# Optimization experiments

Hardware: AMD Instinct MI355X
Metric: run time of the kernel (lower is better)

The kernel has to match this reference:

```python
import jax, jax.numpy as jnp
import numpy as np

B, S, D = 2, 2048, 2048
H, HKV = 32, 8
DH = D // H          # 64
G = H // HKV         # group size 4


def setup_inputs() -> dict:
    key = jax.random.key(0)
    ks = jax.random.split(key, 5)
    sc = lambda fan_in: 1.0 / np.sqrt(fan_in)
    return {
        "hidden_states": jax.random.normal(ks[0], (B, S, D), jnp.float32),
        "Wq": jax.random.normal(ks[1], (D, D), jnp.float32) * sc(D),
        "bq": jnp.zeros((D,), jnp.float32),
        "Wk": jax.random.normal(ks[2], (D, HKV * DH), jnp.float32) * sc(D),
        "bk": jnp.zeros((HKV * DH,), jnp.float32),
        "Wv": jax.random.normal(ks[3], (D, HKV * DH), jnp.float32) * sc(D),
        "bv": jnp.zeros((HKV * DH,), jnp.float32),
        "Wo": jax.random.normal(ks[4], (D, D), jnp.float32) * sc(D),
        "bo": jnp.zeros((D,), jnp.float32),
    }


def reference(hidden_states, Wq, bq, Wk, bk, Wv, bv, Wo, bo):
    x = hidden_states
    # projections
    q = x @ Wq + bq                     # [B,S,D]
    k = x @ Wk + bk                     # [B,S,HKV*DH]
    v = x @ Wv + bv
    # split heads; group queries so K/V broadcast instead of repeat_interleave
    # (same math: repeat_interleave expands kv head j to query heads j*G..j*G+G-1)
    q = q.reshape(B, S, HKV, G, DH).transpose(0, 2, 3, 1, 4)  # [B,HKV,G,S,DH]
    k = k.reshape(B, S, HKV, DH).transpose(0, 2, 1, 3)        # [B,HKV,S,DH]
    v = v.reshape(B, S, HKV, DH).transpose(0, 2, 1, 3)
    scale = 1.0 / jnp.sqrt(jnp.asarray(DH, q.dtype))
    scores = jnp.einsum('bhgqd,bhkd->bhgqk', q, k) * scale    # [B,HKV,G,S,S]
    attn = jax.nn.softmax(scores, axis=-1)
    ctx = jnp.einsum('bhgqk,bhkd->bhgqd', attn, v)            # [B,HKV,G,S,DH]
    # merge heads back to [B,S,D] (head order = kv_head*G + group idx)
    merged = ctx.transpose(0, 3, 1, 2, 4).reshape(B, S, D)
    out = merged @ Wo + bo
    return out
```

## Files before the change

kernel.cpp:

```cpp
#include <hip/hip_runtime.h>
#include <cstdint>

typedef __bf16 bf16;
typedef __attribute__((ext_vector_type(8))) __bf16 bf16x8;
typedef __attribute__((ext_vector_type(4))) __bf16 bf16x4;
typedef __attribute__((ext_vector_type(2))) __bf16 bf16x2;
typedef __attribute__((ext_vector_type(4))) float f32x4;
typedef __attribute__((ext_vector_type(16))) float f32x16;

#define B_   2
#define S_   2048
#define D_   2048
#define HKV_ 8
#define H_   32
#define DH_  64

__device__ __forceinline__ void async_cp16(const bf16* g, bf16* l) {
  __builtin_amdgcn_global_load_lds(
      (__attribute__((address_space(1))) void*)g,
      (__attribute__((address_space(3))) void*)l,
      16, 0, 0);
}

__device__ __forceinline__ float fexp2(float x) {
#if __has_builtin(__builtin_amdgcn_exp2f)
  return __builtin_amdgcn_exp2f(x);
#else
  return __expf(x * 0.69314718056f);
#endif
}

__global__ __launch_bounds__(256) void downcast_k(
    const float* __restrict__ in, bf16* __restrict__ out, int n8) {
  const int i = blockIdx.x * 256 + threadIdx.x;
  if (i < n8) {
    const float4* p = (const float4*)(in + (size_t)i * 8);
    const float4 lo = p[0];
    const float4 hi = p[1];
    bf16x8 v;
    v[0] = (bf16)lo.x; v[1] = (bf16)lo.y; v[2] = (bf16)lo.z; v[3] = (bf16)lo.w;
    v[4] = (bf16)hi.x; v[5] = (bf16)hi.y; v[6] = (bf16)hi.z; v[7] = (bf16)hi.w;
    *(bf16x8*)(out + (size_t)i * 8) = v;
  }
}

__global__ __launch_bounds__(256) void transpose_k(
    const float* __restrict__ in, bf16* __restrict__ out, int R, int C) {
  __shared__ bf16 tile[64][65];
  const int tx = threadIdx.x & 63;
  const int ty = threadIdx.x >> 6;
  const int r0 = blockIdx.x * 64;
  const int c0 = blockIdx.y * 64;
#pragma unroll
  for (int j = 0; j < 16; ++j) {
    int r = j * 4 + ty;
    tile[r][tx] = (bf16)in[(size_t)(r0 + r) * C + c0 + tx];
  }
  __syncthreads();
#pragma unroll
  for (int j = 0; j < 16; ++j) {
    int r = j * 4 + ty;
    out[(size_t)(c0 + r) * R + r0 + tx] = tile[tx][r];
  }
}

template <int OMODE>
__global__ __launch_bounds__(256) void gemm_bt(
    const bf16* __restrict__ A, const bf16* __restrict__ Bt,
    const float* __restrict__ b1, const float* __restrict__ b2,
    const float* __restrict__ b3,
    void* __restrict__ C0, void* __restrict__ C1, void* __restrict__ C2,
    int N, int K) {
  __shared__ bf16 a_tile[128 * 64];
  __shared__ bf16 b_tile[128 * 64];
  const int tid  = threadIdx.x;
  const int wave = tid >> 6;
  const int lane = tid & 63;
  const int quad = lane >> 4;
  const int l16  = lane & 15;
  const int m0   = blockIdx.x * 128;
  const int n0   = blockIdx.y * 128;
  const int wm   = (wave >> 1) * 64;
  const int wn   = (wave & 1) * 64;

  f32x4 acc[4][4] = {};

  const int srow  = wave * 32 + (lane >> 3);
  const int skoff = (lane & 7) * 8;
  const bf16* Ag = A  + (size_t)(m0 + srow) * K + skoff;
  const bf16* Bg = Bt + (size_t)(n0 + srow) * K + skoff;
  bf16* al = &a_tile[srow * 64 + skoff];
  bf16* bl = &b_tile[srow * 64 + skoff];

  for (int kt = 0; kt < K; kt += 64) {
    __syncthreads();
#pragma unroll
    for (int c = 0; c < 4; ++c)
      async_cp16(Ag + (size_t)(c * 8) * K + kt, al + c * 512);
#pragma unroll
    for (int c = 0; c < 4; ++c)
      async_cp16(Bg + (size_t)(c * 8) * K + kt, bl + c * 512);
    __syncthreads();
#pragma unroll
    for (int kk = 0; kk < 64; kk += 32) {
      bf16x8 af[4], bfr[4];
#pragma unroll
      for (int i = 0; i < 4; ++i) {
        af[i]  = *(const bf16x8*)&a_tile[(wm + i * 16 + l16) * 64 + kk + quad * 8];
        bfr[i] = *(const bf16x8*)&b_tile[(wn + i * 16 + l16) * 64 + kk + quad * 8];
      }
#pragma unroll
      for (int i = 0; i < 4; ++i)
#pragma unroll
        for (int j = 0; j < 4; ++j)
          acc[i][j] = __builtin_amdgcn_mfma_f32_16x16x32_bf16(af[i], bfr[j], acc[i][j], 0, 0, 0);
    }
  }

#pragma unroll
  for (int i = 0; i < 4; ++i) {
    const int row = m0 + wm + i * 16 + quad * 4;
#pragma unroll
    for (int j = 0; j < 4; ++j) {
      const int col = n0 + wn + j * 16 + l16;
      if constexpr (OMODE == 2) {
        const float bia = b1[col];
#pragma unroll
        for (int r = 0; r < 4; ++r)
          ((float*)C0)[(size_t)(row + r) * N + col] = acc[i][j][r] + bia;
      } else {
        if (col < 2048) {
          const float bia = b1[col];
#pragma unroll
          for (int r = 0; r < 4; ++r)
            ((bf16*)C0)[(size_t)(row + r) * 2048 + col] =
                (bf16)((acc[i][j][r] + bia) * 0.18033688f);
        } else if (col < 2560) {
          const int cc = col - 2048;
          const float bia = b2[cc];
#pragma unroll
          for (int r = 0; r < 4; ++r)
            ((bf16*)C1)[(size_t)(row + r) * 512 + cc] = (bf16)(acc[i][j][r] + bia);
        } else {
          const int cc = col - 2560;
          const float bia = b3[cc];
          const int hh = cc >> 6, dd = cc & 63;
#pragma unroll
          for (int r = 0; r < 4; ++r) {
            const int rr = row + r;
            const int bb = rr >> 11, ss = rr & 2047;
            ((bf16*)C2)[((((size_t)bb * HKV_ + hh) * DH_ + dd) << 11) + ss] =
                (bf16)(acc[i][j][r] + bia);
          }
        }
      }
    }
  }
}

__global__ __launch_bounds__(256, 2) void gqa_flash(
    const bf16* __restrict__ Qs,
    const bf16* __restrict__ Kb,
    const bf16* __restrict__ VT,
    bf16* __restrict__ ctx) {
  __shared__ bf16 k_tile[2][128 * 64];

  const int tid  = threadIdx.x;
  const int wave = tid >> 6;
  const int lane = tid & 63;
  const int l32  = lane & 31;
  const int hi   = lane >> 5;

  const int qt = blockIdx.x;
  const int hq = blockIdx.y;
  const int b  = blockIdx.z;
  const int h  = hq >> 2;

  const int r2 = (l32 & 7) ^ ((l32 >> 3) & 3);

  bf16x8 qf0[4], qf1[4];
  const int qrow0 = b * S_ + qt * 256 + wave * 64;
  {
    const bf16* qp = Qs + (size_t)(qrow0 + l32) * D_ + hq * DH_ + hi * 8;
#pragma unroll
    for (int ks = 0; ks < 4; ++ks) {
      qf0[ks] = *(const bf16x8*)(qp + ks * 16);
      qf1[ks] = *(const bf16x8*)(qp + (size_t)32 * D_ + ks * 16);
    }
  }

  f32x16 o0[2] = {}, o1[2] = {};
  float l_run0 = 0.f, l_run1 = 0.f;

  const int cg0 = (lane & 7) ^ ((lane >> 3) & 7);
  const bf16* Kg0 = Kb + (size_t)(b * S_ + wave * 32 + (lane >> 3)) * (HKV_ * DH_) + h * DH_;
  const int ldsl = wave * 2048 + lane * 8;

  const bf16* Vrow = VT + ((size_t)(b * HKV_ + h) * DH_ + l32) * S_ + hi * 8;

  auto stage = [&](int buf, int kt0) {
    bf16* kd = &k_tile[0][0] + buf * 8192 + ldsl;
#pragma unroll
    for (int c = 0; c < 4; ++c)
      async_cp16(Kg0 + (size_t)(kt0 + c * 8) * (HKV_ * DH_) + ((cg0 ^ c) << 3),
                 kd + c * 512);
  };

  stage(0, 0);
  __syncthreads();

  for (int kt = 0; kt < S_; kt += 128) {
    stage(((kt >> 7) + 1) & 1, (kt + 128) & (S_ - 1));
    const bf16* ktile = k_tile[(kt >> 7) & 1];

#pragma unroll
    for (int kb = 0; kb < 4; ++kb) {
      f32x16 st0 = {}, st1 = {};
      __builtin_amdgcn_s_setprio(1);
#pragma unroll
      for (int ks = 0; ks < 4; ++ks) {
        bf16x8 kf = *(const bf16x8*)&ktile[(kb * 32 + l32) * 64 +
                                           (((ks * 2 + hi) ^ r2) << 3)];
        st0 = __builtin_amdgcn_mfma_f32_32x32x16_bf16(kf, qf0[ks], st0, 0, 0, 0);
        st1 = __builtin_amdgcn_mfma_f32_32x32x16_bf16(kf, qf1[ks], st1, 0, 0, 0);
      }
      __builtin_amdgcn_s_setprio(0);

      const int koff = kt + kb * 32;
      bf16x8 av00 = *(const bf16x8*)(Vrow + koff);
      bf16x8 av01 = *(const bf16x8*)(Vrow + (size_t)32 * S_ + koff);
      bf16x8 av10 = *(const bf16x8*)(Vrow + koff + 16);
      bf16x8 av11 = *(const bf16x8*)(Vrow + (size_t)32 * S_ + koff + 16);

#pragma unroll
      for (int kqlo = 0; kqlo < 2; ++kqlo) {
        int wa[4], wb[4];
        float sm0 = 0.f, sm1 = 0.f;
#pragma unroll
        for (int e2 = 0; e2 < 4; ++e2) {
          const int e = 4 * kqlo + e2;
          const float a0 = fexp2(st0[2 * e]);
          const float a1 = fexp2(st0[2 * e + 1]);
          sm0 += a0 + a1;
          bf16x2 t0; t0[0] = (bf16)a0; t0[1] = (bf16)a1;
          wa[e2] = __builtin_bit_cast(int, t0);
          const float c0 = fexp2(st1[2 * e]);
          const float c1 = fexp2(st1[2 * e + 1]);
          sm1 += c0 + c1;
          bf16x2 t1; t1[0] = (bf16)c0; t1[1] = (bf16)c1;
          wb[e2] = __builtin_bit_cast(int, t1);
        }
        l_run0 += sm0;
        l_run1 += sm1;

        auto ra0 = __builtin_amdgcn_permlane32_swap(wa[0], wa[2], false, false);
        auto ra1 = __builtin_amdgcn_permlane32_swap(wa[1], wa[3], false, false);
        auto rb0 = __builtin_amdgcn_permlane32_swap(wb[0], wb[2], false, false);
        auto rb1 = __builtin_amdgcn_permlane32_swap(wb[1], wb[3], false, false);
        union { int wi[4]; bf16x8 v; } pb0, pb1;
        pb0.wi[0] = ra0[0]; pb0.wi[1] = ra1[0]; pb0.wi[2] = ra0[1]; pb0.wi[3] = ra1[1];
        pb1.wi[0] = rb0[0]; pb1.wi[1] = rb1[0]; pb1.wi[2] = rb0[1]; pb1.wi[3] = rb1[1];

        const bf16x8 av0 = (kqlo == 0) ? av00 : av10;
        const bf16x8 av1 = (kqlo == 0) ? av01 : av11;
        __builtin_amdgcn_s_setprio(1);
        o0[0] = __builtin_amdgcn_mfma_f32_32x32x16_bf16(av0, pb0.v, o0[0], 0, 0, 0);
        o1[0] = __builtin_amdgcn_mfma_f32_32x32x16_bf16(av0, pb1.v, o1[0], 0, 0, 0);
        o0[1] = __builtin_amdgcn_mfma_f32_32x32x16_bf16(av1, pb0.v, o0[1], 0, 0, 0);
        o1[1] = __builtin_amdgcn_mfma_f32_32x32x16_bf16(av1, pb1.v, o1[1], 0, 0, 0);
        __builtin_amdgcn_s_setprio(0);
      }
    }
    __syncthreads();
  }

  l_run0 += __shfl_xor(l_run0, 32);
  l_run1 += __shfl_xor(l_run1, 32);
  const float inv0 = 1.f / l_run0;
  const float inv1 = 1.f / l_run1;

  const size_t qrowA = (size_t)(qrow0 + l32);
  const size_t qrowB = qrowA + 32;
#pragma unroll
  for (int jm = 0; jm < 2; ++jm)
#pragma unroll
    for (int c = 0; c < 4; ++c) {
      bf16x4 ov;
#pragma unroll
      for (int j = 0; j < 4; ++j) ov[j] = (bf16)(o0[jm][4 * c + j] * inv0);
      const int dh0 = jm * 32 + c * 8 + hi * 4;
      *(bf16x4*)&ctx[qrowA * D_ + hq * DH_ + dh0] = ov;
#pragma unroll
      for (int j = 0; j < 4; ++j) ov[j] = (bf16)(o1[jm][4 * c + j] * inv1);
      *(bf16x4*)&ctx[qrowB * D_ + hq * DH_ + dh0] = ov;
    }
}

extern "C" void kernel_launch(void* const* d_in, const int* in_sizes, int n_in,
                              void* d_out, int out_size, void* d_ws, size_t ws_size,
                              hipStream_t stream) {
  const float* x  = (const float*)d_in[0];
  const float* Wq = (const float*)d_in[1];
  const float* bq = (const float*)d_in[2];
  const float* Wk = (const float*)d_in[3];
  const float* bk = (const float*)d_in[4];
  const float* Wv = (const float*)d_in[5];
  const float* bv = (const float*)d_in[6];
  const float* Wo = (const float*)d_in[7];
  const float* bo = (const float*)d_in[8];
  float* out = (float*)d_out;

  char* ws = (char*)d_ws;
  bf16* WT  = (bf16*)(ws);
  bf16* ctx = (bf16*)(ws);
  bf16* WoT = (bf16*)(ws + 16777216);
  bf16* Qs  = (bf16*)(ws + 25165824);
  bf16* Kb  = (bf16*)(ws + 41943040);
  bf16* VT  = (bf16*)(ws + 46137344);
  bf16* xb  = (bf16*)d_out;

  dim3 blk(256);
  downcast_k<<<dim3(4096), blk, 0, stream>>>(x, xb, (B_ * S_ * D_) / 8);
  transpose_k<<<dim3(32, 32), blk, 0, stream>>>(Wq, WT, 2048, 2048);
  transpose_k<<<dim3(32, 8),  blk, 0, stream>>>(Wk, WT + (size_t)2048 * 2048, 2048, 512);
  transpose_k<<<dim3(32, 8),  blk, 0, stream>>>(Wv, WT + (size_t)2560 * 2048, 2048, 512);
  transpose_k<<<dim3(32, 32), blk, 0, stream>>>(Wo, WoT, 2048, 2048);

  gemm_bt<3><<<dim3(32, 24), blk, 0, stream>>>(
      xb, WT, bq, bk, bv, Qs, Kb, VT, 3072, 2048);

  gqa_flash<<<dim3(8, 32, 2), blk, 0, stream>>>(Qs, Kb, VT, ctx);

  gemm_bt<2><<<dim3(32, 16), blk, 0, stream>>>(
      ctx, WoT, bo, nullptr, nullptr, out, nullptr, nullptr, 2048, 2048);
}
```

Before: 366.7 us.

## Double-buffer GEMM LDS tiles and swizzle workgroup IDs across XCDs

The projection GEMM now keeps two LDS buffers, so the next K-tile's async global-to-LDS loads are issued before computing on the current tile, overlapping memory with MFMA work and dropping one barrier per iteration. Workgroup IDs are also remapped so consecutive blocks land on the same XCD slice, aimed at better L2 reuse. This doubles LDS use to 64KB per block, which may lower occupancy. The async loads are not explicitly waited on before the barrier, so correctness depends on the barrier draining outstanding vmcnt.

```diff
diff --git a/kernel.cpp b/kernel.cpp
--- a/kernel.cpp
+++ b/kernel.cpp
@@ -71,17 +71,20 @@
     const float* __restrict__ b3,
     void* __restrict__ C0, void* __restrict__ C1, void* __restrict__ C2,
     int N, int K) {
-  __shared__ bf16 a_tile[128 * 64];
-  __shared__ bf16 b_tile[128 * 64];
+  __shared__ bf16 a_tile[2][128 * 64];
+  __shared__ bf16 b_tile[2][128 * 64];
   const int tid  = threadIdx.x;
   const int wave = tid >> 6;
   const int lane = tid & 63;
   const int quad = lane >> 4;
   const int l16  = lane & 15;
-  const int m0   = blockIdx.x * 128;
-  const int n0   = blockIdx.y * 128;
-  const int wm   = (wave >> 1) * 64;
-  const int wn   = (wave & 1) * 64;
+
+  const int nwg = gridDim.x * gridDim.y;
+  const int id  = blockIdx.y * gridDim.x + blockIdx.x;
+  const int per = nwg >> 3;
+  const int sw  = (id & 7) * per + (id >> 3);
+  const int m0  = (sw % gridDim.x) * 128;
+  const int n0  = (sw / gridDim.x) * 128;
 
   f32x4 acc[4][4] = {};
 
@@ -89,25 +92,34 @@
   const int skoff = (lane & 7) * 8;
   const bf16* Ag = A  + (size_t)(m0 + srow) * K + skoff;
   const bf16* Bg = Bt + (size_t)(n0 + srow) * K + skoff;
-  bf16* al = &a_tile[srow * 64 + skoff];
-  bf16* bl = &b_tile[srow * 64 + skoff];
+  bf16* al = &a_tile[0][srow * 64 + skoff];
+  bf16* bl = &b_tile[0][srow * 64 + skoff];
+
+  auto stage = [&](int buf, int kt) {
+    const int bo = buf * 8192;
+#pragma unroll
+    for (int c = 0; c < 4; ++c)
+      async_cp16(Ag + (size_t)(c * 8) * K + kt, al + bo + c * 512);
+#pragma unroll
+    for (int c = 0; c < 4; ++c)
+      async_cp16(Bg + (size_t)(c * 8) * K + kt, bl + bo + c * 512);
+  };
+
+  stage(0, 0);
+  __syncthreads();
 
   for (int kt = 0; kt < K; kt += 64) {
-    __syncthreads();
-#pragma unroll
-    for (int c = 0; c < 4; ++c)
-      async_cp16(Ag + (size_t)(c * 8) * K + kt, al + c * 512);
-#pragma unroll
-    for (int c = 0; c < 4; ++c)
-      async_cp16(Bg + (size_t)(c * 8) * K + kt, bl + c * 512);
-    __syncthreads();
+    const int cur = (kt >> 6) & 1;
+    if (kt + 64 < K) stage(cur ^ 1, kt + 64);
+    const bf16* at = &a_tile[cur][0];
+    const bf16* bt = &b_tile[cur][0];
 #pragma unroll
     for (int kk = 0; kk < 64; kk += 32) {
       bf16x8 af[4], bfr[4];
 #pragma unroll
       for (int i = 0; i < 4; ++i) {
-        af[i]  = *(const bf16x8*)&a_tile[(wm + i * 16 + l16) * 64 + kk + quad * 8];
-        bfr[i] = *(const bf16x8*)&b_tile[(wn + i * 16 + l16) * 64 + kk + quad * 8];
+        af[i]  = *(const bf16x8*)&at[((wave >> 1) * 64 + i * 16 + l16) * 64 + kk + quad * 8];
+        bfr[i] = *(const bf16x8*)&bt[((wave & 1) * 64 + i * 16 + l16) * 64 + kk + quad * 8];
       }
 #pragma unroll
       for (int i = 0; i < 4; ++i)
@@ -115,8 +127,11 @@
         for (int j = 0; j < 4; ++j)
           acc[i][j] = __builtin_amdgcn_mfma_f32_16x16x32_bf16(af[i], bfr[j], acc[i][j], 0, 0, 0);
     }
-  }
-
+    __syncthreads();
+  }
+
+  const int wm = (wave >> 1) * 64;
+  const int wn = (wave & 1) * 64;
 #pragma unroll
   for (int i = 0; i < 4; ++i) {
     const int row = m0 + wm + i * 16 + quad * 4;
```

Result: slower. 379.9 us (+3.6%).
